# Performance work log

Measured on AMD Instinct MI355X. Metric: run time of the kernel, lower is better.

The kernel has to match this reference:

```python
import jax, jax.numpy as jnp
import numpy as np

EMBED_DIM = 1024
N_HEAD = 16
D_K = EMBED_DIM // N_HEAD


def setup_inputs() -> dict:
    key = jax.random.key(0)
    kq, kk, kv, kwq, kwk, kwv, kwo = jax.random.split(key, 7)
    B, S, E = 4, 2048, EMBED_DIM
    scale = 1.0 / np.sqrt(E)
    return {
        "Q": jax.random.normal(kq, (B, S, E), dtype=jnp.float32),
        "K": jax.random.normal(kk, (B, S, E), dtype=jnp.float32),
        "V": jax.random.normal(kv, (B, S, E), dtype=jnp.float32),
        "mask": jnp.zeros((1,), dtype=jnp.bool_),  # unused by the module's forward
        "Wq": jax.random.normal(kwq, (E, E), dtype=jnp.float32) * scale,
        "Wk": jax.random.normal(kwk, (E, E), dtype=jnp.float32) * scale,
        "Wv": jax.random.normal(kwv, (E, E), dtype=jnp.float32) * scale,
        "Wo": jax.random.normal(kwo, (E, E), dtype=jnp.float32) * scale,
    }


def reference(Q, K, V, mask, Wq, Wk, Wv, Wo):
    B, S, E = Q.shape
    H, Dk = N_HEAD, D_K
    # Linear projections (torch Linear: x @ W.T), split into heads -> [B,H,S,Dk]
    q = (Q @ Wq.T).reshape(B, S, H, Dk).transpose(0, 2, 1, 3)
    k = (K @ Wk.T).reshape(B, S, H, Dk).transpose(0, 2, 1, 3)
    v = (V @ Wv.T).reshape(B, S, H, Dk).transpose(0, 2, 1, 3)
    # Scaled dot-product attention (no mask is passed in the original forward;
    # dropout is identity in eval mode)
    scores = jnp.einsum("bhqd,bhkd->bhqk", q, k) / jnp.sqrt(jnp.float32(Dk))
    attn = jax.nn.softmax(scores, axis=-1)
    ctx = jnp.einsum("bhqk,bhkd->bhqd", attn, v)  # [B,H,S,Dk]
    ctx = ctx.transpose(0, 2, 1, 3).reshape(B, S, E)
    return ctx @ Wo.T
```

## Files before the change

kernel.cpp:

```cpp
#include <hip/hip_runtime.h>
#include <hip/hip_bf16.h>

#define B_  4
#define S_  2048
#define E_  1024
#define H_  16
#define DK_ 64
#define CSC 0.18033688011112042f

using bf16   = __bf16;
using bf16x8 = __attribute__((ext_vector_type(8))) __bf16;
using f32x4  = __attribute__((ext_vector_type(4))) float;

__device__ __forceinline__ f32x4 mfma16(bf16x8 a, bf16x8 b, f32x4 c) {
    return __builtin_amdgcn_mfma_f32_16x16x32_bf16(a, b, c, 0, 0, 0);
}

__device__ __forceinline__ bf16x8 cvt8(float4 a, float4 b) {
    bf16x8 r;
    r[0] = (bf16)a.x; r[1] = (bf16)a.y; r[2] = (bf16)a.z; r[3] = (bf16)a.w;
    r[4] = (bf16)b.x; r[5] = (bf16)b.y; r[6] = (bf16)b.z; r[7] = (bf16)b.w;
    return r;
}

__device__ __forceinline__ void gl16(const void* g, void* l) {
    __builtin_amdgcn_global_load_lds(
        (const __attribute__((address_space(1))) void*)g,
        (__attribute__((address_space(3))) void*)l, 16, 0, 0);
}

#define SBAR() __builtin_amdgcn_s_barrier()
#define WV6() { asm volatile("s_waitcnt vmcnt(6)" ::: "memory");   \
                __builtin_amdgcn_sched_barrier(0); }
#define WV3() { asm volatile("s_waitcnt vmcnt(3)" ::: "memory");   \
                __builtin_amdgcn_sched_barrier(0); }
#define WV0() { asm volatile("s_waitcnt vmcnt(0)" ::: "memory");   \
                __builtin_amdgcn_sched_barrier(0); }
#define WL0() { asm volatile("s_waitcnt lgkmcnt(0)" ::: "memory"); \
                __builtin_amdgcn_sched_barrier(0); }

__global__ __launch_bounds__(256) void cvt_pair(const float* __restrict__ a,
                                                const float* __restrict__ b,
                                                bf16* __restrict__ da,
                                                bf16* __restrict__ db) {
    const float* s = blockIdx.y ? b : a;
    bf16* d = blockIdx.y ? db : da;
    const size_t i = (size_t)blockIdx.x * 256 + threadIdx.x;
    const float4 u = ((const float4*)s)[i * 2];
    const float4 v = ((const float4*)s)[i * 2 + 1];
    ((bf16x8*)d)[i] = cvt8(u, v);
}

__global__ __launch_bounds__(256) void cvtw3(const float* __restrict__ a,
                                             const float* __restrict__ b,
                                             const float* __restrict__ c,
                                             bf16* __restrict__ d, float s0) {
    const int y = blockIdx.y;
    const float* s = y == 0 ? a : y == 1 ? b : c;
    const float sc = y == 0 ? s0 : 1.f;
    const size_t i = (size_t)blockIdx.x * 256 + threadIdx.x;
    float4 u = ((const float4*)s)[i * 2];
    float4 v = ((const float4*)s)[i * 2 + 1];
    u.x *= sc; u.y *= sc; u.z *= sc; u.w *= sc;
    v.x *= sc; v.y *= sc; v.z *= sc; v.w *= sc;
    ((bf16x8*)(d + (size_t)y * E_ * E_))[i] = cvt8(u, v);
}

template <int MODE>
__global__ __launch_bounds__(512, 2) void gemmr(
    const bf16* __restrict__ Aq, const bf16* __restrict__ Ak,
    const bf16* __restrict__ Av, const bf16* __restrict__ Wb,
    bf16* __restrict__ qws, bf16* __restrict__ kws, bf16* __restrict__ vtws,
    float* __restrict__ fout, int selbase) {
    __shared__ __align__(16) char sm[4 * 24576];

    const int t = threadIdx.x;
    const int lane = t & 63, w = t >> 6;
    const int wm = w >> 2, wn = w & 3;
    const int quad = lane >> 4, l16 = lane & 15;

    int sel, gn;
    if (MODE == 0) {
        sel = selbase + (blockIdx.y >> 2);
        gn = (blockIdx.y & 3) * 256;
    } else {
        sel = 0;
        gn = blockIdx.y * 256;
    }
    const int gm = blockIdx.x * 128;

    const bf16* A = (MODE == 1) ? Aq : (sel == 0 ? Aq : sel == 1 ? Ak : Av);
    const bf16* W = (MODE == 1) ? Wb : Wb + (size_t)sel * E_ * E_;

    const int srow = lane >> 2;
    const int scw  = (lane & 3) ^ ((lane >> 3) & 3);
    const char* gA  = (const char*)(A + (size_t)(gm + w * 16 + srow) * E_) + scw * 16;
    const char* gB0 = (const char*)(W + (size_t)(gn + w * 32 + srow) * E_) + scw * 16;
    const char* gB1 = gB0 + (size_t)16 * E_ * 2;

#define STG(s) {                                                       \
        const int _b = ((s) & 3) * 24576;                              \
        const size_t _k = (size_t)(s) * 64;         \
        gl16(gA + _k, sm + _b + w * 1024);                             \
        gl16(gB0 + _k, sm + _b + 8192 + w * 2048);                     \
        gl16(gB1 + _k, sm + _b + 8192 + w * 2048 + 1024);              \
    }

    bf16x8 Af[4], Bf[4];
#define LDFRAGS(s) {                                                   \
        const int _b = ((s) & 3) * 24576;                              \
        _Pragma("unroll") for (int ms = 0; ms < 4; ++ms) {             \
            const int r = wm * 64 + ms * 16 + l16;                     \
            Af[ms] = *(const bf16x8*)(sm + _b + r * 64 +               \
                                      ((quad ^ ((r >> 1) & 3)) * 16)); \
        }                                                              \
        _Pragma("unroll") for (int ns = 0; ns < 4; ++ns) {             \
            const int r = wn * 64 + ns * 16 + l16;                     \
            Bf[ns] = *(const bf16x8*)(sm + _b + 8192 + r * 64 +        \
                                      ((quad ^ ((r >> 1) & 3)) * 16)); \
        }                                                              \
    }

#define MFMACL() {                                                     \
        __builtin_amdgcn_s_setprio(1);                                 \
        _Pragma("unroll") for (int ms = 0; ms < 4; ++ms)               \
        _Pragma("unroll") for (int ns = 0; ns < 4; ++ns)               \
            acc[ms][ns] = mfma16(Af[ms], Bf[ns], acc[ms][ns]);         \
        __builtin_amdgcn_s_setprio(0);                                 \
    }

    f32x4 acc[4][4];
#pragma unroll
    for (int i = 0; i < 4; ++i)
#pragma unroll
        for (int j = 0; j < 4; ++j) acc[i][j] = f32x4{0.f, 0.f, 0.f, 0.f};

    STG(0); STG(1); STG(2);

    for (int s = 0; s < 29; ++s) {
        WV6();
        SBAR();
        STG(s + 3);
        LDFRAGS(s);
        WL0();
        MFMACL();
    }
    WV6(); SBAR(); LDFRAGS(29); WL0(); MFMACL();
    WV3(); SBAR(); LDFRAGS(30); WL0(); MFMACL();
    WV0(); SBAR(); LDFRAGS(31); WL0(); MFMACL();

#pragma unroll
    for (int ms = 0; ms < 4; ++ms)
#pragma unroll
        for (int ns = 0; ns < 4; ++ns) {
            const int col = gn + wn * 64 + ns * 16 + l16;
            const int row0 = gm + wm * 64 + ms * 16 + quad * 4;
            if (MODE == 1) {
#pragma unroll
                for (int r = 0; r < 4; ++r)
                    fout[(size_t)(row0 + r) * E_ + col] = acc[ms][ns][r];
            } else {
                const int h = col >> 6, d = col & (DK_ - 1);
#pragma unroll
                for (int r = 0; r < 4; ++r) {
                    const int i = row0 + r;
                    const int bb = i >> 11, s = i & (S_ - 1);
                    const float v = acc[ms][ns][r];
                    if (sel == 2)
                        vtws[(((size_t)(bb * H_ + h)) * DK_ + d) * S_ + s] = (bf16)v;
                    else if (sel == 1)
                        kws[(((size_t)(bb * H_ + h)) * S_ + s) * DK_ + d] = (bf16)v;
                    else
                        qws[(((size_t)(bb * H_ + h)) * S_ + s) * DK_ + d] = (bf16)v;
                }
            }
        }
#undef STG
#undef LDFRAGS
#undef MFMACL
}

#define PSTR 72
__global__ __launch_bounds__(256) void attn4(const bf16* __restrict__ q,
                                             const bf16* __restrict__ k,
                                             const bf16* __restrict__ vt,
                                             bf16* __restrict__ ctx) {
    __shared__ __align__(16) bf16 sK[64 * 64];
    __shared__ __align__(16) bf16 sV[64 * 64];
    __shared__ __align__(16) bf16 plds[4][32 * PSTR];

    const int t = threadIdx.x;
    const int lane = t & 63, wave = t >> 6;
    const int quad = lane >> 4, l16 = lane & 15;
    const int qb = (blockIdx.x * 4 + wave) * 32;
    const int bh = blockIdx.y;
    const size_t base  = (size_t)bh * S_ * DK_;
    const size_t baseT = (size_t)bh * DK_ * S_;
    bf16* pw = &plds[wave][0];

    const int srow = t >> 2, sc4 = (t & 3) * 16;
    const int cb = (t & 3) * 2, swr = srow & 7;
    const bf16* gK = k + base + (size_t)srow * DK_ + sc4;
    const bf16* gV = vt + baseT + (size_t)srow * S_ + sc4;
    char* wK0 = (char*)sK + srow * 128 + ((cb ^ swr) * 16);
    char* wK1 = (char*)sK + srow * 128 + (((cb + 1) ^ swr) * 16);
    char* wV0 = (char*)sV + srow * 128 + ((cb ^ swr) * 16);
    char* wV1 = (char*)sV + srow * 128 + (((cb + 1) ^ swr) * 16);

    bf16x8 rk[2], rv[2];
    rk[0] = *(const bf16x8*)(gK);
    rk[1] = *(const bf16x8*)(gK + 8);
    rv[0] = *(const bf16x8*)(gV);
    rv[1] = *(const bf16x8*)(gV + 8);

    bf16x8 aQ[2][2];
#pragma unroll
    for (int t2 = 0; t2 < 2; ++t2) {
        const bf16* qp = q + base + (size_t)(qb + t2 * 16 + l16) * DK_ + quad * 8;
        aQ[t2][0] = *(const bf16x8*)(qp);
        aQ[t2][1] = *(const bf16x8*)(qp + 32);
    }

    f32x4 acc[2][4];
    float l_i[2][4];
#pragma unroll
    for (int t2 = 0; t2 < 2; ++t2)
#pragma unroll
        for (int nb = 0; nb < 4; ++nb) {
            acc[t2][nb] = f32x4{0.f, 0.f, 0.f, 0.f};
            l_i[t2][nb] = 0.f;
        }

    for (int kt = 0; kt < S_ / 64; ++kt) {
        __syncthreads();
        *(bf16x8*)wK0 = rk[0];
        *(bf16x8*)wK1 = rk[1];
        *(bf16x8*)wV0 = rv[0];
        *(bf16x8*)wV1 = rv[1];
        __syncthreads();
        if (kt + 1 < S_ / 64) {
            const bf16* nK = gK + (size_t)(kt + 1) * 64 * DK_;
            const bf16* nV = gV + (size_t)(kt + 1) * 64;
            rk[0] = *(const bf16x8*)(nK);
            rk[1] = *(const bf16x8*)(nK + 8);
            rv[0] = *(const bf16x8*)(nV);
            rv[1] = *(const bf16x8*)(nV + 8);
        }

        f32x4 sc[2][4];
#pragma unroll
        for (int kb = 0; kb < 4; ++kb) {
            const int r = kb * 16 + l16, sw = r & 7;
            const bf16x8 b0 =
                *(const bf16x8*)((const char*)sK + r * 128 + ((quad ^ sw) * 16));
            const bf16x8 b1 = *(const bf16x8*)((const char*)sK + r * 128 +
                                               (((quad + 4) ^ sw) * 16));
#pragma unroll
            for (int t2 = 0; t2 < 2; ++t2) {
                f32x4 z = f32x4{0.f, 0.f, 0.f, 0.f};
                z = mfma16(aQ[t2][0], b0, z);
                sc[t2][kb] = mfma16(aQ[t2][1], b1, z);
            }
        }

#pragma unroll
        for (int t2 = 0; t2 < 2; ++t2)
#pragma unroll
            for (int r = 0; r < 4; ++r) {
                const int prow = (t2 * 16 + quad * 4 + r) * PSTR;
#pragma unroll
                for (int kb = 0; kb < 4; ++kb) {
                    const float p = __builtin_amdgcn_exp2f(sc[t2][kb][r]);
                    l_i[t2][r] += p;
                    pw[prow + kb * 16 + l16] = (bf16)p;
                }
            }

        bf16x8 aP[2][2];
#pragma unroll
        for (int t2 = 0; t2 < 2; ++t2) {
            aP[t2][0] = *(const bf16x8*)(pw + (t2 * 16 + l16) * PSTR + quad * 8);
            aP[t2][1] = *(const bf16x8*)(pw + (t2 * 16 + l16) * PSTR + 32 + quad * 8);
        }

#pragma unroll
        for (int nb = 0; nb < 4; ++nb) {
            const int r = nb * 16 + l16, sw = r & 7;
            const bf16x8 b0 =
                *(const bf16x8*)((const char*)sV + r * 128 + ((quad ^ sw) * 16));
            const bf16x8 b1 = *(const bf16x8*)((const char*)sV + r * 128 +
                                               (((quad + 4) ^ sw) * 16));
#pragma unroll
            for (int t2 = 0; t2 < 2; ++t2) {
                acc[t2][nb] = mfma16(aP[t2][0], b0, acc[t2][nb]);
                acc[t2][nb] = mfma16(aP[t2][1], b1, acc[t2][nb]);
            }
        }
    }

#pragma unroll
    for (int t2 = 0; t2 < 2; ++t2)
#pragma unroll
        for (int r = 0; r < 4; ++r) {
            float x = l_i[t2][r];
            x += __shfl_xor(x, 1);
            x += __shfl_xor(x, 2);
            x += __shfl_xor(x, 4);
            x += __shfl_xor(x, 8);
            l_i[t2][r] = 1.f / x;
        }

    const int b = bh >> 4, h = bh & (H_ - 1);
#pragma unroll
    for (int t2 = 0; t2 < 2; ++t2)
#pragma unroll
        for (int nb = 0; nb < 4; ++nb)
#pragma unroll
            for (int r = 0; r < 4; ++r) {
                const int s = qb + t2 * 16 + quad * 4 + r;
                const size_t idx =
                    ((size_t)(b * S_ + s)) * E_ + h * DK_ + nb * 16 + l16;
                ctx[idx] = (bf16)(acc[t2][nb][r] * l_i[t2][r]);
            }
}

extern "C" void kernel_launch(void* const* d_in, const int* in_sizes, int n_in,
                              void* d_out, int out_size, void* d_ws,
                              size_t ws_size, hipStream_t stream) {
    const float* Q  = (const float*)d_in[0];
    const float* K  = (const float*)d_in[1];
    const float* V  = (const float*)d_in[2];
    const float* Wq = (const float*)d_in[4];
    const float* Wk = (const float*)d_in[5];
    const float* Wv = (const float*)d_in[6];
    const float* Wo = (const float*)d_in[7];
    float* out = (float*)d_out;

    const size_t NTOK = (size_t)B_ * S_ * E_;
    bf16* qws  = (bf16*)d_ws;
    bf16* kws  = qws + NTOK;
    bf16* vtws = kws + NTOK;
    bf16* cws  = vtws + NTOK;

    bf16* wqkvb = cws;
    bf16* wob   = qws;
    bf16* Qb = (bf16*)d_out;
    bf16* Kb = Qb + NTOK;
    bf16* Vb = Qb;

    cvt_pair<<<dim3(4096, 2), 256, 0, stream>>>(Q, K, Qb, Kb);
    cvtw3<<<dim3(512, 3), 256, 0, stream>>>(Wq, Wk, Wv, wqkvb, CSC);

    gemmr<0><<<dim3(64, 8), 512, 0, stream>>>(
        Qb, Kb, Vb, wqkvb, qws, kws, vtws, nullptr, 0);

    cvt_pair<<<dim3(4096, 1), 256, 0, stream>>>(V, V, Vb, Vb);

    gemmr<0><<<dim3(64, 4), 512, 0, stream>>>(
        Qb, Kb, Vb, wqkvb, qws, kws, vtws, nullptr, 2);

    attn4<<<dim3(S_ / 128, B_ * H_), 256, 0, stream>>>(qws, kws, vtws, cws);

    cvtw3<<<dim3(512, 1), 256, 0, stream>>>(Wo, Wo, Wo, wob, 1.f);

    gemmr<1><<<dim3(64, 4), 512, 0, stream>>>(
        cws, cws, cws, wob, nullptr, nullptr, nullptr, out, 0);
}
```

Measured before the change: 384.4 us.

## Use 3-stage GEMM pipeline for occupancy; transpose attention scores for vectorized P stores

The projection GEMM drops from four to three LDS stages, which lowers shared memory per block, and raises launch bounds to target four blocks per CU. The prefetch depth and waitcnt values are adjusted to match, with a rotating buffer index. The attention kernel now computes S^T by swapping MFMA operands, so each lane holds four consecutive keys. This lets it write P to LDS as swizzled bf16x4 stores and keep one row-sum per tile instead of four, which reduces the shuffle reduction. The trade-off is a shallower prefetch in the GEMM and tighter register limits that could cause spills.

```diff
diff --git a/kernel.cpp b/kernel.cpp
--- a/kernel.cpp
+++ b/kernel.cpp
@@ -9,6 +9,7 @@
 #define CSC 0.18033688011112042f
 
 using bf16   = __bf16;
+using bf16x4 = __attribute__((ext_vector_type(4))) __bf16;
 using bf16x8 = __attribute__((ext_vector_type(8))) __bf16;
 using f32x4  = __attribute__((ext_vector_type(4))) float;
 
@@ -30,8 +31,6 @@
 }
 
 #define SBAR() __builtin_amdgcn_s_barrier()
-#define WV6() { asm volatile("s_waitcnt vmcnt(6)" ::: "memory");   \
-                __builtin_amdgcn_sched_barrier(0); }
 #define WV3() { asm volatile("s_waitcnt vmcnt(3)" ::: "memory");   \
                 __builtin_amdgcn_sched_barrier(0); }
 #define WV0() { asm volatile("s_waitcnt vmcnt(0)" ::: "memory");   \
@@ -67,12 +66,12 @@
 }
 
 template <int MODE>
-__global__ __launch_bounds__(512, 2) void gemmr(
+__global__ __launch_bounds__(512, 4) void gemmr(
     const bf16* __restrict__ Aq, const bf16* __restrict__ Ak,
     const bf16* __restrict__ Av, const bf16* __restrict__ Wb,
     bf16* __restrict__ qws, bf16* __restrict__ kws, bf16* __restrict__ vtws,
     float* __restrict__ fout, int selbase) {
-    __shared__ __align__(16) char sm[4 * 24576];
+    __shared__ __align__(16) char sm[3 * 24576];
 
     const int t = threadIdx.x;
     const int lane = t & 63, w = t >> 6;
@@ -98,25 +97,23 @@
     const char* gB0 = (const char*)(W + (size_t)(gn + w * 32 + srow) * E_) + scw * 16;
     const char* gB1 = gB0 + (size_t)16 * E_ * 2;
 
-#define STG(s) {                                                       \
-        const int _b = ((s) & 3) * 24576;                              \
+#define STG(bb, s) {                                                   \
         const size_t _k = (size_t)(s) * 64;         \
-        gl16(gA + _k, sm + _b + w * 1024);                             \
-        gl16(gB0 + _k, sm + _b + 8192 + w * 2048);                     \
-        gl16(gB1 + _k, sm + _b + 8192 + w * 2048 + 1024);              \
+        gl16(gA + _k, sm + (bb) + w * 1024);                           \
+        gl16(gB0 + _k, sm + (bb) + 8192 + w * 2048);                   \
+        gl16(gB1 + _k, sm + (bb) + 8192 + w * 2048 + 1024);            \
     }
 
     bf16x8 Af[4], Bf[4];
-#define LDFRAGS(s) {                                                   \
-        const int _b = ((s) & 3) * 24576;                              \
+#define LDFRAGS(bb) {                                                  \
         _Pragma("unroll") for (int ms = 0; ms < 4; ++ms) {             \
             const int r = wm * 64 + ms * 16 + l16;                     \
-            Af[ms] = *(const bf16x8*)(sm + _b + r * 64 +               \
+            Af[ms] = *(const bf16x8*)(sm + (bb) + r * 64 +             \
                                       ((quad ^ ((r >> 1) & 3)) * 16)); \
         }                                                              \
         _Pragma("unroll") for (int ns = 0; ns < 4; ++ns) {             \
             const int r = wn * 64 + ns * 16 + l16;                     \
-            Bf[ns] = *(const bf16x8*)(sm + _b + 8192 + r * 64 +        \
+            Bf[ns] = *(const bf16x8*)(sm + (bb) + 8192 + r * 64 +      \
                                       ((quad ^ ((r >> 1) & 3)) * 16)); \
         }                                                              \
     }
@@ -135,19 +132,22 @@
 #pragma unroll
         for (int j = 0; j < 4; ++j) acc[i][j] = f32x4{0.f, 0.f, 0.f, 0.f};
 
-    STG(0); STG(1); STG(2);
-
-    for (int s = 0; s < 29; ++s) {
-        WV6();
+    STG(0, 0); STG(24576, 1);
+
+    int bc = 0, bs = 2 * 24576;
+    for (int s = 0; s < 30; ++s) {
+        WV3();
         SBAR();
-        STG(s + 3);
-        LDFRAGS(s);
+        STG(bs, s + 2);
+        LDFRAGS(bc);
         WL0();
         MFMACL();
-    }
-    WV6(); SBAR(); LDFRAGS(29); WL0(); MFMACL();
-    WV3(); SBAR(); LDFRAGS(30); WL0(); MFMACL();
-    WV0(); SBAR(); LDFRAGS(31); WL0(); MFMACL();
+        bc += 24576; if (bc == 73728) bc = 0;
+        bs += 24576; if (bs == 73728) bs = 0;
+    }
+    WV3(); SBAR(); LDFRAGS(bc); WL0(); MFMACL();
+    bc += 24576; if (bc == 73728) bc = 0;
+    WV0(); SBAR(); LDFRAGS(bc); WL0(); MFMACL();
 
 #pragma unroll
     for (int ms = 0; ms < 4; ++ms)
@@ -180,14 +180,13 @@
 #undef MFMACL
 }
 
-#define PSTR 72
 __global__ __launch_bounds__(256) void attn4(const bf16* __restrict__ q,
                                              const bf16* __restrict__ k,
                                              const bf16* __restrict__ vt,
                                              bf16* __restrict__ ctx) {
     __shared__ __align__(16) bf16 sK[64 * 64];
     __shared__ __align__(16) bf16 sV[64 * 64];
-    __shared__ __align__(16) bf16 plds[4][32 * PSTR];
+    __shared__ __align__(16) bf16 pP[4][32 * 64];
 
     const int t = threadIdx.x;
     const int lane = t & 63, wave = t >> 6;
@@ -196,7 +195,7 @@
     const int bh = blockIdx.y;
     const size_t base  = (size_t)bh * S_ * DK_;
     const size_t baseT = (size_t)bh * DK_ * S_;
-    bf16* pw = &plds[wave][0];
+    char* pwb = (char*)&pP[wave][0];
 
     const int srow = t >> 2, sc4 = (t & 3) * 16;
     const int cb = (t & 3) * 2, swr = srow & 7;
@@ -222,14 +221,11 @@
     }
 
     f32x4 acc[2][4];
-    float l_i[2][4];
+    float l_i[2] = {0.f, 0.f};
 #pragma unroll
     for (int t2 = 0; t2 < 2; ++t2)
 #pragma unroll
-        for (int nb = 0; nb < 4; ++nb) {
-            acc[t2][nb] = f32x4{0.f, 0.f, 0.f, 0.f};
-            l_i[t2][nb] = 0.f;
-        }
+        for (int nb = 0; nb < 4; ++nb) acc[t2][nb] = f32x4{0.f, 0.f, 0.f, 0.f};
 
     for (int kt = 0; kt < S_ / 64; ++kt) {
         __syncthreads();
@@ -247,7 +243,7 @@
             rv[1] = *(const bf16x8*)(nV + 8);
         }
 
-        f32x4 sc[2][4];
+        f32x4 scT[2][4];
 #pragma unroll
         for (int kb = 0; kb < 4; ++kb) {
             const int r = kb * 16 + l16, sw = r & 7;
@@ -258,29 +254,37 @@
 #pragma unroll
             for (int t2 = 0; t2 < 2; ++t2) {
                 f32x4 z = f32x4{0.f, 0.f, 0.f, 0.f};
-                z = mfma16(aQ[t2][0], b0, z);
-                sc[t2][kb] = mfma16(aQ[t2][1], b1, z);
-            }
-        }
-
-#pragma unroll
-        for (int t2 = 0; t2 < 2; ++t2)
-#pragma unroll
-            for (int r = 0; r < 4; ++r) {
-                const int prow = (t2 * 16 + quad * 4 + r) * PSTR;
-#pragma unroll
-                for (int kb = 0; kb < 4; ++kb) {
-                    const float p = __builtin_amdgcn_exp2f(sc[t2][kb][r]);
-                    l_i[t2][r] += p;
-                    pw[prow + kb * 16 + l16] = (bf16)p;
-                }
-            }
+                z = mfma16(b0, aQ[t2][0], z);
+                scT[t2][kb] = mfma16(b1, aQ[t2][1], z);
+            }
+        }
+
+#pragma unroll
+        for (int t2 = 0; t2 < 2; ++t2) {
+            const int prow = (t2 * 16 + l16) * 128;
+#pragma unroll
+            for (int kb = 0; kb < 4; ++kb) {
+                const float p0 = __builtin_amdgcn_exp2f(scT[t2][kb][0]);
+                const float p1 = __builtin_amdgcn_exp2f(scT[t2][kb][1]);
+                const float p2 = __builtin_amdgcn_exp2f(scT[t2][kb][2]);
+                const float p3 = __builtin_amdgcn_exp2f(scT[t2][kb][3]);
+                l_i[t2] += (p0 + p1) + (p2 + p3);
+                bf16x4 pv;
+                pv[0] = (bf16)p0; pv[1] = (bf16)p1;
+                pv[2] = (bf16)p2; pv[3] = (bf16)p3;
+                *(bf16x4*)(pwb + prow +
+                           (((2 * kb + (quad >> 1)) ^ (l16 & 7)) * 16) +
+                           (quad & 1) * 8) = pv;
+            }
+        }
 
         bf16x8 aP[2][2];
 #pragma unroll
         for (int t2 = 0; t2 < 2; ++t2) {
-            aP[t2][0] = *(const bf16x8*)(pw + (t2 * 16 + l16) * PSTR + quad * 8);
-            aP[t2][1] = *(const bf16x8*)(pw + (t2 * 16 + l16) * PSTR + 32 + quad * 8);
+            const int prow = (t2 * 16 + l16) * 128;
+            aP[t2][0] = *(const bf16x8*)(pwb + prow + (((quad) ^ (l16 & 7)) * 16));
+            aP[t2][1] =
+                *(const bf16x8*)(pwb + prow + (((4 + quad) ^ (l16 & 7)) * 16));
         }
 
 #pragma unroll
@@ -298,30 +302,29 @@
         }
     }
 
+    float linv[2];
+#pragma unroll
+    for (int t2 = 0; t2 < 2; ++t2) {
+        float x = l_i[t2];
+        x += __shfl_xor(x, 16);
+        x += __shfl_xor(x, 32);
+        linv[t2] = 1.f / x;
+    }
+
+    const int b = bh >> 4, h = bh & (H_ - 1);
 #pragma unroll
     for (int t2 = 0; t2 < 2; ++t2)
 #pragma unroll
         for (int r = 0; r < 4; ++r) {
-            float x = l_i[t2][r];
-            x += __shfl_xor(x, 1);
-            x += __shfl_xor(x, 2);
-            x += __shfl_xor(x, 4);
-            x += __shfl_xor(x, 8);
-            l_i[t2][r] = 1.f / x;
-        }
-
-    const int b = bh >> 4, h = bh & (H_ - 1);
-#pragma unroll
-    for (int t2 = 0; t2 < 2; ++t2)
-#pragma unroll
-        for (int nb = 0; nb < 4; ++nb)
-#pragma unroll
-            for (int r = 0; r < 4; ++r) {
-                const int s = qb + t2 * 16 + quad * 4 + r;
+            const float li = __shfl(linv[t2], quad * 4 + r);
+            const int s = qb + t2 * 16 + quad * 4 + r;
+#pragma unroll
+            for (int nb = 0; nb < 4; ++nb) {
                 const size_t idx =
                     ((size_t)(b * S_ + s)) * E_ + h * DK_ + nb * 16 + l16;
-                ctx[idx] = (bf16)(acc[t2][nb][r] * l_i[t2][r]);
-            }
+                ctx[idx] = (bf16)(acc[t2][nb][r] * li);
+            }
+        }
 }
 
 extern "C" void kernel_launch(void* const* d_in, const int* in_sizes, int n_in,
```

Result: faster. 339.6 us (-11.7%).
